# Kernel tuning notes

Hardware: AMD Instinct MI355X
Metric: run time of the kernel (lower is better)

The kernel has to match this reference:

```python
import jax, jax.numpy as jnp
import numpy as np

TEMPERATURE = 10.0
N_CLASSES = 10


def _sqdist(a, b):
    # squared euclidean distances, [Na, Nb] == torch.cdist(a, b) ** 2
    an = jnp.sum(a * a, axis=1)[:, None]
    bn = jnp.sum(b * b, axis=1)[None, :]
    return jnp.maximum(an + bn - 2.0 * (a @ b.T), 0.0)


def setup_inputs() -> dict:
    key = jax.random.key(0)
    ks = jax.random.split(key, 6)
    B, N, D, H, C = 512, 4096, 512, 2048, N_CLASSES
    return {
        "x": jax.random.normal(ks[0], (B, D), dtype=jnp.float32),
        "star_features": jax.random.normal(ks[1], (N, D), dtype=jnp.float32),
        "from_features": jax.random.normal(ks[2], (N, D), dtype=jnp.float32),
        "star_label_ids": jax.random.randint(ks[3], (N,), 0, C),
        "W1": jax.random.normal(ks[4], (D, H), dtype=jnp.float32) * 0.02,
        "b1": jnp.zeros((H,), dtype=jnp.float32),
        "W2": jax.random.normal(ks[5], (H, C), dtype=jnp.float32) * 0.02,
        "b2": jnp.zeros((C,), dtype=jnp.float32),
    }


def _transport_features(x, feats_to, star_feats):
    # dists: [N_star, B]
    d = _sqdist(star_feats, x)
    d = d / jnp.mean(d, axis=0, keepdims=True)
    e = jnp.exp(-TEMPERATURE * d)                    # [N_star, B]
    w = feats_to.T @ e                               # [d_to, B]
    return (w / jnp.sum(e, axis=0, keepdims=True)).T  # [B, d_to]


def reference(x, star_features, from_features, star_label_ids, W1, b1, W2, b2):
    B = x.shape[0]
    C = N_CLASSES
    # --- exact-match lookup against dataset_star features (fused eq+all reduce) ---
    mask = jnp.all(x[:, None, :] == star_features[None, :, :], axis=2)  # [B, N_star]
    matched = jnp.any(mask, axis=1)                                      # [B]
    match_idx = jnp.argmax(mask, axis=1)                                 # [B]
    # --- transport features: matched samples take aligned dataset sample, rest use OT map ---
    xt_unmatched = _transport_features(x, from_features, star_features)  # [B, d]
    xt_matched = from_features[match_idx]                                # [B, d]
    x_transported = jnp.where(matched[:, None], xt_matched, xt_unmatched)
    # --- run the model in the transported domain (MLP classifier) ---
    h = jax.nn.relu(x_transported @ W1 + b1)
    logits = h @ W2 + b2                                                 # [B, C]
    # --- project_labels: preds and one-hot unique labels have equal dim -> cdist/argmin branch ---
    unique_labels = jnp.eye(C, dtype=logits.dtype)
    closest = jnp.argmin(_sqdist(logits, unique_labels), axis=1)
    y_proj = unique_labels[closest]                                      # [B, C] (unused by 'all_features')
    # --- transport_labels, method='all_features': feature-distance-weighted average of star labels ---
    d2 = _sqdist(from_features, x_transported)                           # [N_from, B]
    d2 = d2 / jnp.mean(d2, axis=0, keepdims=True)
    e2 = jnp.exp(-TEMPERATURE * d2)
    star_labels = jax.nn.one_hot(star_label_ids, C, dtype=x.dtype)       # [N_star, C]
    y_star = (star_labels.T @ e2 / jnp.sum(e2, axis=0, keepdims=True)).T  # [B, C]
    # single (model, dataset) pair -> sum/len is identity
    return y_star
```

## Files before the change

kernel.cpp:

```cpp
#include <hip/hip_runtime.h>

#define TEMP 10.0f
#define NS 4096
#define BB 512
#define DDIM 512
#define NCLS 10
#define LDSP 72

typedef short bf16x8 __attribute__((ext_vector_type(8)));
typedef float f32x4 __attribute__((ext_vector_type(4)));

__device__ inline short f2bf(float f) {
    unsigned u = __builtin_bit_cast(unsigned, f);
    u += 0x7FFFu + ((u >> 16) & 1u);
    return (short)(u >> 16);
}
__device__ inline float bf2f(short h) {
    unsigned u = ((unsigned)(unsigned short)h) << 16;
    return __builtin_bit_cast(float, u);
}

__device__ inline float block_sum(float s, float* red) {
    #pragma unroll
    for (int off = 32; off > 0; off >>= 1) s += __shfl_down(s, off);
    int wid = threadIdx.x >> 6;
    if ((threadIdx.x & 63) == 0) red[wid] = s;
    __syncthreads();
    float tot = red[0] + red[1] + red[2] + red[3];
    __syncthreads();
    return tot;
}

__global__ __launch_bounds__(256)
void prep(const float* __restrict__ x, const float* __restrict__ star,
          const float* __restrict__ from,
          short* __restrict__ Xb, short* __restrict__ Sb,
          short* __restrict__ FTb, short* __restrict__ Fb,
          float* __restrict__ xn2, float* __restrict__ sn2, float* __restrict__ fn2,
          float* __restrict__ scol, float* __restrict__ xcol, int* __restrict__ midx,
          float* __restrict__ spart, float* __restrict__ fpart)
{
    __shared__ short tile[64][LDSP];
    int bid = blockIdx.x, t = threadIdx.x;
    if (bid < 2176) {
        const float* in; short* outb; float* n2; float* colb; float* part; int rowbase;
        if (bid < 1024)      { in = star; outb = Sb; n2 = sn2; colb = scol; rowbase = bid * 4;
                               part = spart + (size_t)bid * 512; }
        else if (bid < 1152) { in = x;    outb = Xb; n2 = xn2; colb = xcol; rowbase = (bid - 1024) * 4;
                               part = nullptr; }
        else                 { in = from; outb = Fb; n2 = fn2; colb = nullptr; rowbase = (bid - 1152) * 4;
                               part = fpart + (size_t)(bid - 1152) * 512; }
        if (bid == 1024) { midx[t] = NS; midx[256 + t] = NS; }
        int w = t >> 6;
        int row = rowbase + w;
        int l = t & 63;
        const float4* p = (const float4*)(in + (size_t)row * DDIM) + l * 2;
        float4 a = p[0], b = p[1];
        float s = a.x*a.x + a.y*a.y + a.z*a.z + a.w*a.w
                + b.x*b.x + b.y*b.y + b.z*b.z + b.w*b.w;
        bf16x8 h;
        h[0]=f2bf(a.x); h[1]=f2bf(a.y); h[2]=f2bf(a.z); h[3]=f2bf(a.w);
        h[4]=f2bf(b.x); h[5]=f2bf(b.y); h[6]=f2bf(b.z); h[7]=f2bf(b.w);
        *(bf16x8*)(outb + (size_t)row * DDIM + l * 8) = h;
        #pragma unroll
        for (int off = 32; off > 0; off >>= 1) s += __shfl_down(s, off);
        if (l == 0) {
            n2[row] = s;
            if (colb) colb[row] = a.x;
        }
        if (part) {
            float* cp = (float*)tile;
            *(float4*)&cp[w * 512 + l * 8]     = a;
            *(float4*)&cp[w * 512 + l * 8 + 4] = b;
            __syncthreads();
            int c = t * 2;
            float2 o;
            o.x = cp[c]     + cp[512 + c]     + cp[1024 + c]     + cp[1536 + c];
            o.y = cp[c + 1] + cp[512 + c + 1] + cp[1024 + c + 1] + cp[1536 + c + 1];
            *(float2*)&part[c] = o;
        }
        return;
    }
    int tid2 = bid - 2176;
    int n0 = (tid2 & 63) * 64, d0 = (tid2 >> 6) * 64;
    int r = t >> 4, c4 = (t & 15) * 4;
    #pragma unroll
    for (int rr = 0; rr < 64; rr += 16) {
        float4 v = *(const float4*)(from + (size_t)(n0 + r + rr) * DDIM + d0 + c4);
        tile[r + rr][c4 + 0] = f2bf(v.x);
        tile[r + rr][c4 + 1] = f2bf(v.y);
        tile[r + rr][c4 + 2] = f2bf(v.z);
        tile[r + rr][c4 + 3] = f2bf(v.w);
    }
    __syncthreads();
    int dr = t >> 2, nco = (t & 3) * 16;
    short tmp[16];
    #pragma unroll
    for (int q = 0; q < 16; ++q) tmp[q] = tile[nco + q][dr];
    short* op = FTb + (size_t)(d0 + dr) * NS + n0 + nco;
    *(bf16x8*)op       = *(bf16x8*)tmp;
    *(bf16x8*)(op + 8) = *(bf16x8*)(tmp + 8);
}

__global__ __launch_bounds__(256)
void finmatch(const float* __restrict__ spart, const float* __restrict__ fpart,
              const float* __restrict__ sn2, const float* __restrict__ fn2,
              float* __restrict__ sbar, float* __restrict__ fbar,
              float* __restrict__ sms, float* __restrict__ fms,
              const float* __restrict__ x, const float* __restrict__ star,
              const float* __restrict__ scol, const float* __restrict__ xcol,
              int* __restrict__ midx)
{
    int bid = blockIdx.x, t = threadIdx.x;
    if (bid < 32) {
        __shared__ float red2[8][33];
        int m = bid & 1;
        int c0 = (bid >> 1) * 32;
        const float* part = m ? fpart : spart;
        float* outm = m ? fbar : sbar;
        int c = c0 + (t & 31);
        int p0 = (t >> 5) * 128;
        float s = 0.f;
        #pragma unroll 8
        for (int p = 0; p < 128; ++p)
            s += part[(size_t)(p0 + p) * 512 + c];
        red2[t >> 5][t & 31] = s;
        __syncthreads();
        if (t < 32) {
            float tot = 0.f;
            #pragma unroll
            for (int q = 0; q < 8; ++q) tot += red2[q][t];
            outm[c0 + t] = tot * (1.0f / NS);
        }
        return;
    }
    if (bid < 34) {
        __shared__ float red[4];
        int m = bid - 32;
        const float* n2v = m ? fn2 : sn2;
        float* outs = m ? fms : sms;
        float s = 0.f;
        #pragma unroll
        for (int q = 0; q < 16; ++q) s += n2v[q * 256 + t];
        float tot = block_sum(s, red);
        if (t == 0) outs[0] = tot * (1.0f / NS);
        return;
    }
    __shared__ float xl[BB];
    *(float2*)&xl[t * 2] = *(const float2*)&xcol[t * 2];
    __syncthreads();
    int n = (bid - 34) * 256 + t;
    float sv = scol[n];
    #pragma unroll 4
    for (int b4 = 0; b4 < BB; b4 += 4) {
        float4 xv = *(const float4*)&xl[b4];
        if (xv.x == sv || xv.y == sv || xv.z == sv || xv.w == sv) {
            #pragma unroll
            for (int j = 0; j < 4; ++j) {
                int b = b4 + j;
                if (xl[b] == sv) {
                    const float* xr = x + (size_t)b * DDIM;
                    const float* sr = star + (size_t)n * DDIM;
                    bool eq = true;
                    for (int k = 0; k < DDIM && eq; k += 4) {
                        float4 a = *(const float4*)(xr + k);
                        float4 c4v = *(const float4*)(sr + k);
                        eq = (a.x == c4v.x) && (a.y == c4v.y) &&
                             (a.z == c4v.z) && (a.w == c4v.w);
                    }
                    if (eq) atomicMin(&midx[b], n);
                }
            }
        }
    }
}

__global__ __launch_bounds__(256)
void esc1k(const float* __restrict__ x, const float* __restrict__ sbar,
           const float* __restrict__ sms, const float* __restrict__ xn2,
           float* __restrict__ escale1)
{
    int t = threadIdx.x;
    int lane = t & 63, w = t >> 6;
    int b = blockIdx.x * 4 + w;
    const float4* xp = (const float4*)(x + (size_t)b * DDIM) + lane * 2;
    const float4* sp = (const float4*)sbar + lane * 2;
    float4 xa = xp[0], xb = xp[1], sa = sp[0], sb = sp[1];
    float dot = xa.x*sa.x + xa.y*sa.y + xa.z*sa.z + xa.w*sa.w
              + xb.x*sb.x + xb.y*sb.y + xb.z*sb.z + xb.w*sb.w;
    #pragma unroll
    for (int m = 32; m > 0; m >>= 1) dot += __shfl_xor(dot, m);
    if (lane == 0)
        escale1[b] = -TEMP / (sms[0] + xn2[b] - 2.0f * dot);
}

template<int WSE>
__global__ __launch_bounds__(256)
void gemm_exp(const short* __restrict__ A, const short* __restrict__ B,
              const float* __restrict__ an2, const float* __restrict__ bn2,
              const float* __restrict__ escale, short* __restrict__ Eout,
              float* __restrict__ sumEp, int nt)
{
    __shared__ short As[2][64][LDSP];
    __shared__ short Bs[2][64][LDSP];
    __shared__ float se[2][64];
    const int K = DDIM;
    int t = threadIdx.x;
    int m0 = blockIdx.x * 64;
    int n0 = blockIdx.y * 64;
    int wid = t >> 6, lane = t & 63;
    int wr = wid >> 1, wc = wid & 1;
    int lr = lane & 15, lk = lane >> 4;

    int ar = t >> 2, ak = (t & 3) * 16;
    const short* Ag = A + (size_t)(m0 + ar) * K + ak;
    const short* Bg = B + (size_t)(n0 + ar) * K + ak;

    f32x4 acc[2][2] = {};
    bf16x8 ra0 = *(const bf16x8*)Ag;
    bf16x8 ra1 = *(const bf16x8*)(Ag + 8);
    bf16x8 rb0 = *(const bf16x8*)Bg;
    bf16x8 rb1 = *(const bf16x8*)(Bg + 8);
    int cur = 0;
    *(bf16x8*)&As[0][ar][ak]     = ra0;
    *(bf16x8*)&As[0][ar][ak + 8] = ra1;
    *(bf16x8*)&Bs[0][ar][ak]     = rb0;
    *(bf16x8*)&Bs[0][ar][ak + 8] = rb1;

    for (int it = 0; it < nt; ++it) {
        __syncthreads();
        if (it + 1 < nt) {
            int ko = (it + 1) * 64;
            ra0 = *(const bf16x8*)(Ag + ko);
            ra1 = *(const bf16x8*)(Ag + ko + 8);
            rb0 = *(const bf16x8*)(Bg + ko);
            rb1 = *(const bf16x8*)(Bg + ko + 8);
        }
        #pragma unroll
        for (int ks = 0; ks < 2; ++ks) {
            int k0 = ks * 32 + lk * 8;
            bf16x8 af[2], bfr[2];
            #pragma unroll
            for (int i = 0; i < 2; ++i)
                af[i] = *(const bf16x8*)&As[cur][wr * 32 + i * 16 + lr][k0];
            #pragma unroll
            for (int j = 0; j < 2; ++j)
                bfr[j] = *(const bf16x8*)&Bs[cur][wc * 32 + j * 16 + lr][k0];
            #pragma unroll
            for (int i = 0; i < 2; ++i)
                #pragma unroll
                for (int j = 0; j < 2; ++j)
                    acc[i][j] = __builtin_amdgcn_mfma_f32_16x16x32_bf16(
                        af[i], bfr[j], acc[i][j], 0, 0, 0);
        }
        if (it + 1 < nt) {
            cur ^= 1;
            *(bf16x8*)&As[cur][ar][ak]     = ra0;
            *(bf16x8*)&As[cur][ar][ak + 8] = ra1;
            *(bf16x8*)&Bs[cur][ar][ak]     = rb0;
            *(bf16x8*)&Bs[cur][ar][ak + 8] = rb1;
        }
    }
    float bn2v[2];
    int gnv[2];
    #pragma unroll
    for (int j = 0; j < 2; ++j) { gnv[j] = n0 + wc * 32 + j * 16 + lr; bn2v[j] = bn2[gnv[j]]; }
    #pragma unroll
    for (int i = 0; i < 2; ++i) {
        #pragma unroll
        for (int r = 0; r < 4; ++r) {
            int gm = m0 + wr * 32 + i * 16 + lk * 4 + r;
            float a2 = an2[gm];
            float sc = escale[gm];
            float rs = 0.f;
            #pragma unroll
            for (int j = 0; j < 2; ++j) {
                float dv = fmaxf(a2 + bn2v[j] - 2.0f * acc[i][j][r], 0.0f);
                short hb = f2bf(__expf(dv * sc));
                Eout[(size_t)gm * NS + gnv[j]] = hb;
                if (WSE) rs += bf2f(hb);
            }
            if (WSE) {
                #pragma unroll
                for (int m = 1; m < 16; m <<= 1) rs += __shfl_xor(rs, m);
                if (lr == 0) se[wc][wr * 32 + i * 16 + lk * 4 + r] = rs;
            }
        }
    }
    if (WSE) {
        __syncthreads();
        if (t < 64)
            sumEp[(size_t)(m0 + t) * 64 + blockIdx.y] = se[0][t] + se[1][t];
    }
}

__global__ __launch_bounds__(512)
void gemm_bt8(const short* __restrict__ A, const short* __restrict__ B, int K,
              int kslab, int nt, float* __restrict__ C, int ldc, size_t cstride)
{
    __shared__ short As[2][64][LDSP];
    __shared__ short Bs[2][128][LDSP];
    int t = threadIdx.x;
    int m0 = blockIdx.x * 64;
    int n0 = blockIdx.y * 128;
    int kbase = blockIdx.z * kslab;
    float* Cp = C + (size_t)blockIdx.z * cstride;
    int wid = t >> 6, lane = t & 63;
    int wr = wid >> 2, wc = wid & 3;
    int lr = lane & 15, lk = lane >> 4;

    int ar = t >> 3, ak = (t & 7) * 8;
    int br = t >> 2, bk = (t & 3) * 16;
    const short* Ag = A + (size_t)(m0 + ar) * K + kbase + ak;
    const short* Bg = B + (size_t)(n0 + br) * K + kbase + bk;

    f32x4 acc[2][2] = {};
    bf16x8 ra0 = *(const bf16x8*)Ag;
    bf16x8 rb0 = *(const bf16x8*)Bg;
    bf16x8 rb1 = *(const bf16x8*)(Bg + 8);
    int cur = 0;
    *(bf16x8*)&As[0][ar][ak]     = ra0;
    *(bf16x8*)&Bs[0][br][bk]     = rb0;
    *(bf16x8*)&Bs[0][br][bk + 8] = rb1;

    for (int it = 0; it < nt; ++it) {
        __syncthreads();
        if (it + 1 < nt) {
            int ko = (it + 1) * 64;
            ra0 = *(const bf16x8*)(Ag + ko);
            rb0 = *(const bf16x8*)(Bg + ko);
            rb1 = *(const bf16x8*)(Bg + ko + 8);
        }
        #pragma unroll
        for (int ks = 0; ks < 2; ++ks) {
            int k0 = ks * 32 + lk * 8;
            bf16x8 af[2], bfr[2];
            #pragma unroll
            for (int i = 0; i < 2; ++i)
                af[i] = *(const bf16x8*)&As[cur][wr * 32 + i * 16 + lr][k0];
            #pragma unroll
            for (int j = 0; j < 2; ++j)
                bfr[j] = *(const bf16x8*)&Bs[cur][wc * 32 + j * 16 + lr][k0];
            #pragma unroll
            for (int i = 0; i < 2; ++i)
                #pragma unroll
                for (int j = 0; j < 2; ++j)
                    acc[i][j] = __builtin_amdgcn_mfma_f32_16x16x32_bf16(
                        af[i], bfr[j], acc[i][j], 0, 0, 0);
        }
        if (it + 1 < nt) {
            cur ^= 1;
            *(bf16x8*)&As[cur][ar][ak]     = ra0;
            *(bf16x8*)&Bs[cur][br][bk]     = rb0;
            *(bf16x8*)&Bs[cur][br][bk + 8] = rb1;
        }
    }
    #pragma unroll
    for (int i = 0; i < 2; ++i) {
        #pragma unroll
        for (int r = 0; r < 4; ++r) {
            int gm = m0 + wr * 32 + i * 16 + lk * 4 + r;
            #pragma unroll
            for (int j = 0; j < 2; ++j) {
                int gn = n0 + wc * 32 + j * 16 + lr;
                Cp[(size_t)gm * ldc + gn] = acc[i][j][r];
            }
        }
    }
}

__global__ __launch_bounds__(256)
void xt_fin(const float* __restrict__ wpart, const float* __restrict__ sumEp,
            const int* __restrict__ midx, const float* __restrict__ fromf,
            const float* __restrict__ fbar, const float* __restrict__ fms,
            short* __restrict__ xtb, float* __restrict__ xtn2,
            float* __restrict__ escale2)
{
    __shared__ float red[4];
    int b = blockIdx.x;
    int t = threadIdx.x;
    int d = t * 2;
    int mi = midx[b];
    float sv = (t < 64) ? sumEp[(size_t)b * 64 + t] : 0.f;
    float stot = block_sum(sv, red);
    float inv = 1.0f / stot;
    float v0 = 0.f, v1 = 0.f;
    #pragma unroll
    for (int sl = 0; sl < 8; ++sl) {
        float2 p = *(const float2*)(wpart + (size_t)sl * (BB * DDIM) + (size_t)b * DDIM + d);
        v0 += p.x; v1 += p.y;
    }
    v0 *= inv; v1 *= inv;
    if (mi < NS) {
        v0 = fromf[(size_t)mi * DDIM + d];
        v1 = fromf[(size_t)mi * DDIM + d + 1];
    }
    xtb[(size_t)b * DDIM + d]     = f2bf(v0);
    xtb[(size_t)b * DDIM + d + 1] = f2bf(v1);
    float nt2 = block_sum(v0 * v0 + v1 * v1, red);
    float2 fb2 = *(const float2*)(fbar + d);
    float fd = block_sum(v0 * fb2.x + v1 * fb2.y, red);
    if (t == 0) {
        xtn2[b] = nt2;
        escale2[b] = -TEMP / (fms[0] + nt2 - 2.0f * fd);
    }
}

__global__ __launch_bounds__(256)
void ystar_fin(const short* __restrict__ e2T, const int* __restrict__ labels,
               float* __restrict__ out)
{
    __shared__ float cred[NCLS + 1][4];
    int b = blockIdx.x;
    int t = threadIdx.x;
    const short* row = e2T + (size_t)b * NS + t * 16;
    bf16x8 h0 = *(const bf16x8*)row;
    bf16x8 h1 = *(const bf16x8*)(row + 8);
    float accs[NCLS] = {};
    float te = 0.f;
    #pragma unroll
    for (int q = 0; q < 4; ++q) {
        int4 lb = *(const int4*)(labels + t * 16 + q * 4);
        int lbl[4] = {lb.x, lb.y, lb.z, lb.w};
        #pragma unroll
        for (int e = 0; e < 4; ++e) {
            int idx = q * 4 + e;
            float ev = bf2f(idx < 8 ? h0[idx] : h1[idx - 8]);
            te += ev;
            #pragma unroll
            for (int c = 0; c < NCLS; ++c) accs[c] += (lbl[e] == c) ? ev : 0.f;
        }
    }
    int wid = t >> 6, lane = t & 63;
    #pragma unroll
    for (int c = 0; c < NCLS + 1; ++c) {
        float sv = (c < NCLS) ? accs[c] : te;
        #pragma unroll
        for (int off = 32; off > 0; off >>= 1) sv += __shfl_down(sv, off);
        if (lane == 0) cred[c][wid] = sv;
    }
    __syncthreads();
    if (t < NCLS) {
        float num = cred[t][0] + cred[t][1] + cred[t][2] + cred[t][3];
        float den = cred[NCLS][0] + cred[NCLS][1] + cred[NCLS][2] + cred[NCLS][3];
        out[b * NCLS + t] = num / den;
    }
}

extern "C" void kernel_launch(void* const* d_in, const int* in_sizes, int n_in,
                              void* d_out, int out_size, void* d_ws, size_t ws_size,
                              hipStream_t stream) {
    const float* x     = (const float*)d_in[0];
    const float* star  = (const float*)d_in[1];
    const float* from  = (const float*)d_in[2];
    const int*   label = (const int*)d_in[3];
    float* out = (float*)d_out;

    float* F = (float*)d_ws;
    float* wpart = F;
    short* Sb    = (short*)(F + 2097152);
    short* FTb   = (short*)(F + 3145728);
    short* Fb    = (short*)(F + 4194304);
    short* Eb    = (short*)(F + 5242880);
    short* E2b   = (short*)(F + 6291456);
    short* Xb    = (short*)(F + 7340032);
    short* XTb   = (short*)(F + 7471104);
    float* sn2   = F + 7602176;
    float* fn2   = F + 7606272;
    float* xn2   = F + 7610368;
    float* xtn2  = F + 7610880;
    float* esc1  = F + 7611392;
    float* esc2  = F + 7611904;
    float* sbar  = F + 7612416;
    float* fbar  = F + 7612928;
    float* sms   = F + 7613440;
    float* fms   = F + 7613456;
    float* sumEp = F + 7613472;
    float* scol  = F + 7646240;
    float* xcol  = F + 7650336;
    int*   midx  = (int*)(F + 7650848);
    float* spart = F + 7651360;
    float* fpart = F + 8175648;

    prep<<<2688, 256, 0, stream>>>(x, star, from, Xb, Sb, FTb, Fb,
                                   xn2, sn2, fn2, scol, xcol, midx, spart, fpart);
    finmatch<<<50, 256, 0, stream>>>(spart, fpart, sn2, fn2, sbar, fbar, sms, fms,
                                     x, star, scol, xcol, midx);
    esc1k<<<128, 256, 0, stream>>>(x, sbar, sms, xn2, esc1);
    gemm_exp<1><<<dim3(8, 64), 256, 0, stream>>>(Xb, Sb, xn2, sn2, esc1, Eb, sumEp, 8);
    gemm_bt8<<<dim3(8, 4, 8), 512, 0, stream>>>(Eb, FTb, NS, 512, 8, wpart, DDIM,
                                                (size_t)BB * DDIM);
    xt_fin<<<BB, 256, 0, stream>>>(wpart, sumEp, midx, from, fbar, fms,
                                   XTb, xtn2, esc2);
    gemm_exp<0><<<dim3(8, 64), 256, 0, stream>>>(XTb, Fb, xtn2, fn2, esc2, E2b, nullptr, 8);
    ystar_fin<<<BB, 256, 0, stream>>>(E2b, label, out);
}
```

Baseline: 68.93 us.

## Fuse label-weighted reduction into second exp GEMM epilogue, drop E2 matrix

The second distance GEMM now reduces its exp values per class inside the epilogue, using labels staged in shared memory. It writes per-tile class partial sums instead of storing the full bf16 exp matrix. A small kernel sums the 64 partials per row and normalizes, which removes a 4 MB write and read of E2. In exchange the epilogue gains shared-memory staging, extra barriers, more LDS use per block, and fp32 rather than bf16-rounded exp values.

```diff
diff --git a/kernel.cpp b/kernel.cpp
--- a/kernel.cpp
+++ b/kernel.cpp
@@ -194,16 +194,20 @@
         escale1[b] = -TEMP / (sms[0] + xn2[b] - 2.0f * dot);
 }
 
-template<int WSE>
+template<int MODE>
 __global__ __launch_bounds__(256)
 void gemm_exp(const short* __restrict__ A, const short* __restrict__ B,
               const float* __restrict__ an2, const float* __restrict__ bn2,
               const float* __restrict__ escale, short* __restrict__ Eout,
-              float* __restrict__ sumEp, int nt)
+              float* __restrict__ sumEp, const int* __restrict__ labels,
+              float* __restrict__ ybin, int nt)
 {
     __shared__ short As[2][64][LDSP];
     __shared__ short Bs[2][64][LDSP];
     __shared__ float se[2][64];
+    __shared__ float esum[64][65];
+    __shared__ float ybq[64][4][NCLS];
+    __shared__ int lbl_l[64];
     const int K = DDIM;
     int t = threadIdx.x;
     int m0 = blockIdx.x * 64;
@@ -226,6 +230,7 @@
     *(bf16x8*)&As[0][ar][ak + 8] = ra1;
     *(bf16x8*)&Bs[0][ar][ak]     = rb0;
     *(bf16x8*)&Bs[0][ar][ak + 8] = rb1;
+    if (MODE == 2 && t < 64) lbl_l[t] = labels[n0 + t];
 
     for (int it = 0; it < nt; ++it) {
         __syncthreads();
@@ -269,28 +274,63 @@
     for (int i = 0; i < 2; ++i) {
         #pragma unroll
         for (int r = 0; r < 4; ++r) {
-            int gm = m0 + wr * 32 + i * 16 + lk * 4 + r;
+            int lrow = wr * 32 + i * 16 + lk * 4 + r;
+            int gm = m0 + lrow;
             float a2 = an2[gm];
             float sc = escale[gm];
             float rs = 0.f;
             #pragma unroll
             for (int j = 0; j < 2; ++j) {
                 float dv = fmaxf(a2 + bn2v[j] - 2.0f * acc[i][j][r], 0.0f);
-                short hb = f2bf(__expf(dv * sc));
-                Eout[(size_t)gm * NS + gnv[j]] = hb;
-                if (WSE) rs += bf2f(hb);
+                float ev = __expf(dv * sc);
+                if (MODE == 1) {
+                    short hb = f2bf(ev);
+                    Eout[(size_t)gm * NS + gnv[j]] = hb;
+                    rs += bf2f(hb);
+                } else {
+                    esum[lrow][wc * 32 + j * 16 + lr] = ev;
+                }
             }
-            if (WSE) {
+            if (MODE == 1) {
                 #pragma unroll
                 for (int m = 1; m < 16; m <<= 1) rs += __shfl_xor(rs, m);
-                if (lr == 0) se[wc][wr * 32 + i * 16 + lk * 4 + r] = rs;
+                if (lr == 0) se[wc][lrow] = rs;
             }
         }
     }
-    if (WSE) {
+    if (MODE == 1) {
         __syncthreads();
         if (t < 64)
             sumEp[(size_t)(m0 + t) * 64 + blockIdx.y] = se[0][t] + se[1][t];
+    } else {
+        __syncthreads();
+        {
+            int row = t >> 2, q = t & 3;
+            float accs[NCLS] = {};
+            #pragma unroll
+            for (int c = 0; c < 16; ++c) {
+                int col = q * 16 + c;
+                float ev = esum[row][col];
+                int lb = lbl_l[col];
+                #pragma unroll
+                for (int cc = 0; cc < NCLS; ++cc) accs[cc] += (lb == cc) ? ev : 0.f;
+            }
+            #pragma unroll
+            for (int cc = 0; cc < NCLS; ++cc) ybq[row][q][cc] = accs[cc];
+        }
+        __syncthreads();
+        if (t < 64) {
+            float o[NCLS];
+            #pragma unroll
+            for (int cc = 0; cc < NCLS; ++cc)
+                o[cc] = ybq[t][0][cc] + ybq[t][1][cc] + ybq[t][2][cc] + ybq[t][3][cc];
+            float* dst = ybin + ((size_t)blockIdx.y * BB + (m0 + t)) * NCLS;
+            #pragma unroll
+            for (int q2 = 0; q2 < NCLS; q2 += 2) {
+                float2 v; v.x = o[q2]; v.y = o[q2 + 1];
+                *(float2*)(dst + q2) = v;
+            }
+        }
     }
 }
 
@@ -407,43 +447,32 @@
 }
 
 __global__ __launch_bounds__(256)
-void ystar_fin(const short* __restrict__ e2T, const int* __restrict__ labels,
-               float* __restrict__ out)
-{
-    __shared__ float cred[NCLS + 1][4];
-    int b = blockIdx.x;
-    int t = threadIdx.x;
-    const short* row = e2T + (size_t)b * NS + t * 16;
-    bf16x8 h0 = *(const bf16x8*)row;
-    bf16x8 h1 = *(const bf16x8*)(row + 8);
-    float accs[NCLS] = {};
-    float te = 0.f;
-    #pragma unroll
-    for (int q = 0; q < 4; ++q) {
-        int4 lb = *(const int4*)(labels + t * 16 + q * 4);
-        int lbl[4] = {lb.x, lb.y, lb.z, lb.w};
-        #pragma unroll
-        for (int e = 0; e < 4; ++e) {
-            int idx = q * 4 + e;
-            float ev = bf2f(idx < 8 ? h0[idx] : h1[idx - 8]);
-            te += ev;
-            #pragma unroll
-            for (int c = 0; c < NCLS; ++c) accs[c] += (lbl[e] == c) ? ev : 0.f;
-        }
-    }
-    int wid = t >> 6, lane = t & 63;
-    #pragma unroll
-    for (int c = 0; c < NCLS + 1; ++c) {
-        float sv = (c < NCLS) ? accs[c] : te;
-        #pragma unroll
-        for (int off = 32; off > 0; off >>= 1) sv += __shfl_down(sv, off);
-        if (lane == 0) cred[c][wid] = sv;
+void ystar_red(const float* __restrict__ ybin, float* __restrict__ out)
+{
+    __shared__ float p[64][NCLS + 2];
+    __shared__ float nums[NCLS];
+    int b = blockIdx.x, t = threadIdx.x;
+    if (t < 64) {
+        const float* src = ybin + ((size_t)t * BB + b) * NCLS;
+        #pragma unroll
+        for (int q = 0; q < NCLS; q += 2) {
+            float2 v = *(const float2*)(src + q);
+            p[t][q] = v.x; p[t][q + 1] = v.y;
+        }
     }
     __syncthreads();
     if (t < NCLS) {
-        float num = cred[t][0] + cred[t][1] + cred[t][2] + cred[t][3];
-        float den = cred[NCLS][0] + cred[NCLS][1] + cred[NCLS][2] + cred[NCLS][3];
-        out[b * NCLS + t] = num / den;
+        float s = 0.f;
+        #pragma unroll 8
+        for (int k = 0; k < 64; ++k) s += p[k][t];
+        nums[t] = s;
+    }
+    __syncthreads();
+    if (t < NCLS) {
+        float den = 0.f;
+        #pragma unroll
+        for (int c = 0; c < NCLS; ++c) den += nums[c];
+        out[b * NCLS + t] = nums[t] / den;
     }
 }
 
@@ -462,7 +491,7 @@
     short* FTb   = (short*)(F + 3145728);
     short* Fb    = (short*)(F + 4194304);
     short* Eb    = (short*)(F + 5242880);
-    short* E2b   = (short*)(F + 6291456);
+    float* ybin  = F + 6291456;
     short* Xb    = (short*)(F + 7340032);
     short* XTb   = (short*)(F + 7471104);
     float* sn2   = F + 7602176;
@@ -487,11 +516,13 @@
     finmatch<<<50, 256, 0, stream>>>(spart, fpart, sn2, fn2, sbar, fbar, sms, fms,
                                      x, star, scol, xcol, midx);
     esc1k<<<128, 256, 0, stream>>>(x, sbar, sms, xn2, esc1);
-    gemm_exp<1><<<dim3(8, 64), 256, 0, stream>>>(Xb, Sb, xn2, sn2, esc1, Eb, sumEp, 8);
+    gemm_exp<1><<<dim3(8, 64), 256, 0, stream>>>(Xb, Sb, xn2, sn2, esc1, Eb, sumEp,
+                                                 nullptr, nullptr, 8);
     gemm_bt8<<<dim3(8, 4, 8), 512, 0, stream>>>(Eb, FTb, NS, 512, 8, wpart, DDIM,
                                                 (size_t)BB * DDIM);
     xt_fin<<<BB, 256, 0, stream>>>(wpart, sumEp, midx, from, fbar, fms,
                                    XTb, xtn2, esc2);
-    gemm_exp<0><<<dim3(8, 64), 256, 0, stream>>>(XTb, Fb, xtn2, fn2, esc2, E2b, nullptr, 8);
-    ystar_fin<<<BB, 256, 0, stream>>>(E2b, label, out);
-}
+    gemm_exp<2><<<dim3(8, 64), 256, 0, stream>>>(XTb, Fb, xtn2, fn2, esc2, nullptr,
+                                                 nullptr, label, ybin, 8);
+    ystar_red<<<BB, 256, 0, stream>>>(ybin, out);
+}
```

New measurement: 67.77 us (median of 2 runs). About the same (-1.7%).
